# Kernel optimization log

Hardware: AMD Instinct MI355X
Metric: run time of the kernel (lower is better)

Reference implementation:

```python
import jax, jax.numpy as jnp
import numpy as np

# ---- fixed analysis filters (pywt_coeffs) ----
GL = np.array([0.05441584224308161, 0.3128715909144659, 0.6756307362980128, 0.5853546836548691, -0.015829105256023893, -0.2840155429624281, 0.00047248457399797254, 0.128747426620186, -0.01736930100202211, -0.04408825393106472, 0.013981027917015516, 0.008746094047015655, -0.00487035299301066, -0.0003917403729959771, 0.0006754494059985568, -0.00011747678400228192])
GH = np.array([-0.00011747678400228192, -0.0006754494059985568, -0.0003917403729959771, 0.00487035299301066, 0.008746094047015655, -0.013981027917015516, -0.04408825393106472, 0.01736930100202211, 0.128747426620186, -0.00047248457399797254, -0.2840155429624281, 0.015829105256023893, 0.5853546836548691, -0.6756307362980128, 0.3128715909144659, -0.05441584224308161])

M2 = 8          # fix(16*0.5), half filter length
A_CUBIC = -0.75 # PyTorch bicubic coefficient


def _ihilbert(x):
    # scipy.fftpack.ihilbert: Fourier coeff y_j = -1j*sign(j)*x_j, y_0 = 0
    n = x.shape[0]
    signs = np.sign(np.fft.fftfreq(n))
    return np.real(np.fft.ifft(np.fft.fft(x) * (-1j) * signs))


def setup_inputs() -> dict:
    key = jax.random.key(0)
    k1, k2 = jax.random.split(key)
    LL = jax.random.normal(k1, (8, 32, 256, 256), dtype=jnp.float32)
    Yh0 = jax.random.normal(k2, (8, 32, 3, 256, 256), dtype=jnp.float32)
    gl = jnp.asarray(GL, dtype=jnp.float32)
    gh = jnp.asarray(GH, dtype=jnp.float32)
    fl = jnp.asarray(_ihilbert(GL), dtype=jnp.float32)
    fh = jnp.asarray(_ihilbert(GH), dtype=jnp.float32)
    return {"LL": LL, "Yh0": Yh0, "gl": gl, "gh": gh, "fl": fl, "fh": fh}


def _reflect_idx(n):
    # reflect(arange(-m2, n+m2), -0.5, n-0.5) -> half-sample reflected indices, length n+2*M2
    x = jnp.arange(-M2, n + M2, dtype=jnp.float32)
    rng = jnp.float32(n)  # (n-0.5) - (-0.5)
    mod = jnp.mod(x + 0.5, 2.0 * rng)
    out = jnp.where(mod >= rng, 2.0 * rng - mod, mod) - 0.5
    return out.astype(jnp.int32)


def colfilter(X, h):
    # Faithful to original: reflect-pad gather along rows, then the original
    # _column_convolve accumulates X*h[idx] WITHOUT shifting (source bug), which
    # equals X_ext * sum(h); the centered crop recovers the original rows.
    r = X.shape[2]
    xe = _reflect_idx(r)
    Y = X[:, :, xe, :] * jnp.sum(h)
    return Y[:, :, M2:M2 + r, :]


def rowfilter(X, h):
    c = X.shape[3]
    xe = _reflect_idx(c)
    Y = X[:, :, :, xe] * jnp.sum(h)
    return Y[:, :, :, M2:M2 + c]


def _cubic_kernel(d):
    d = jnp.abs(d)
    w1 = ((A_CUBIC + 2.0) * d - (A_CUBIC + 3.0)) * d * d + 1.0
    w2 = ((A_CUBIC * d - 5.0 * A_CUBIC) * d + 8.0 * A_CUBIC) * d - 4.0 * A_CUBIC
    return jnp.where(d <= 1.0, w1, jnp.where(d < 2.0, w2, 0.0))


def _up2_axis(X, axis):
    # PyTorch nn.Upsample(scale_factor=2, mode='bicubic', align_corners=False)
    n = X.shape[axis]
    i = jnp.arange(2 * n, dtype=jnp.float32)
    src = 0.5 * i - 0.25                      # (i+0.5)*in/out - 0.5
    f = jnp.floor(src)
    offs = jnp.arange(-1, 3, dtype=jnp.float32)
    pos = f[:, None] + offs[None, :]          # [2n, 4] tap positions
    idx = jnp.clip(pos, 0, n - 1).astype(jnp.int32)
    w = _cubic_kernel(src[:, None] - pos)     # [2n, 4]
    Xg = jnp.take(X, idx.reshape(-1), axis=axis)
    new_shape = X.shape[:axis] + (2 * n, 4) + X.shape[axis + 1:]
    Xg = Xg.reshape(new_shape)
    wb = w.reshape((1,) * axis + (2 * n, 4) + (1,) * (X.ndim - axis - 1))
    return jnp.sum(Xg * wb, axis=axis + 1)


def upsample2(X):
    return _up2_axis(_up2_axis(X, 2), 3)


def _iqwt(LL, Yh0, gl, gh, fl, fh):
    LH, HL, HH = Yh0[:, :, 0], Yh0[:, :, 1], Yh0[:, :, 2]
    s = LL.shape[1] // 4
    sp = lambda T: (T[:, 0:s], T[:, s:2 * s], T[:, 2 * s:3 * s], T[:, 3 * s:4 * s])
    lglg, lflg, lglf, lflf = sp(LL)
    lghg, lfhg, lghf, lfhf = sp(LH)
    hglg, hflg, hglf, hflf = sp(HL)
    hghg, hfhg, hghf, hfhf = sp(HH)

    # first component
    lghg_f = rowfilter(lghg, gh)  # reused below (original code bug)
    t = upsample2(rowfilter(lglg, gl)) + upsample2(lghg_f)
    t1 = colfilter(t, gl)
    t = upsample2(rowfilter(hglg, gl)) + upsample2(rowfilter(hghg, gh))
    first = t1 + colfilter(t, gh)

    # second component (note: original uses lghg_f, not rowfilter(lfhg, gh))
    t = upsample2(rowfilter(lflg, gl)) + upsample2(lghg_f)
    t1 = colfilter(t, fl)
    t = upsample2(rowfilter(hflg, gl)) + upsample2(rowfilter(hfhg, gh))
    second = t1 + colfilter(t, fh)

    # third component
    t = upsample2(rowfilter(lglf, fl)) + upsample2(rowfilter(lghf, fh))
    t1 = colfilter(t, gl)
    t = upsample2(rowfilter(hglf, fl)) + upsample2(rowfilter(hghf, fh))
    third = t1 + colfilter(t, gh)

    # fourth component
    t = upsample2(rowfilter(lflf, fl)) + upsample2(rowfilter(lfhf, fh))
    t1 = colfilter(t, fl)
    t = upsample2(rowfilter(hflf, fl)) + upsample2(rowfilter(hfhf, fh))
    fourth = t1 + colfilter(t, fh)

    y = first + second + third + fourth
    return (y - jnp.min(y)) / (jnp.max(y) - jnp.min(y))


def reference(LL, Yh0, gl, gh, fl, fh):
    return _iqwt(LL, Yh0, gl, gh, fl, fh)
```

## Files before the change

kernel.cpp:

```cpp
#include <hip/hip_runtime.h>

constexpr int IT  = 36;
constexpr int ITP = 37;
constexpr int STP = 68;

#define W0 (-0.03515625f)
#define W1 ( 0.26171875f)
#define W2 ( 0.87890625f)
#define W3 (-0.10546875f)

typedef float vfloat4 __attribute__((ext_vector_type(4)));

template <typename F>
__device__ __forceinline__ void tile_pipeline(
    const float* __restrict__ src, int tx, int ty, int t,
    float (&sIn)[IT][ITP], float (&sT)[IT][STP],
    float a0, float a1, float a2, float a3, int b0, int g, F&& consume)
{
    const int rin0 = ty * 32 - 2;
    const int cin0 = tx * 32 - 2;

    for (int idx = t; idx < IT * IT; idx += 256) {
        int r  = idx / IT;
        int cc = idx - r * IT;
        int gr = min(max(rin0 + r, 0), 255);
        int gc = min(max(cin0 + cc, 0), 255);
        sIn[r][cc] = src[gr * 256 + gc];
    }
    __syncthreads();

    for (int r = t >> 4; r < IT; r += 16) {
        float x0 = sIn[r][2 * g + 0];
        float x1 = sIn[r][2 * g + 1];
        float x2 = sIn[r][2 * g + 2];
        float x3 = sIn[r][2 * g + 3];
        float x4 = sIn[r][2 * g + 4];
        float x5 = sIn[r][2 * g + 5];
        vfloat4 v;
        v.x = W0 * x0 + W1 * x1 + W2 * x2 + W3 * x3;
        v.y = W3 * x1 + W2 * x2 + W1 * x3 + W0 * x4;
        v.z = W0 * x1 + W1 * x2 + W2 * x3 + W3 * x4;
        v.w = W3 * x2 + W2 * x3 + W1 * x4 + W0 * x5;
        *(vfloat4*)&sT[r][4 * g] = v;
    }
    __syncthreads();

#pragma unroll
    for (int it = 0; it < 4; ++it) {
        const int base = b0 + 8 * it;
        vfloat4 q0 = *(const vfloat4*)&sT[base + 0][4 * g];
        vfloat4 q1 = *(const vfloat4*)&sT[base + 1][4 * g];
        vfloat4 q2 = *(const vfloat4*)&sT[base + 2][4 * g];
        vfloat4 q3 = *(const vfloat4*)&sT[base + 3][4 * g];
        vfloat4 v = a0 * q0 + a1 * q1 + a2 * q2 + a3 * q3;
        consume(it, v);
    }
}

__device__ __forceinline__ void block_minmax(int t, float& mn, float& mx) {
    for (int off = 32; off > 0; off >>= 1) {
        mn = fminf(mn, __shfl_down(mn, off, 64));
        mx = fmaxf(mx, __shfl_down(mx, off, 64));
    }
    __shared__ float wmn[4], wmx[4];
    const int wv = t >> 6;
    if ((t & 63) == 0) { wmn[wv] = mn; wmx[wv] = mx; }
    __syncthreads();
    mn = fminf(fminf(wmn[0], wmn[1]), fminf(wmn[2], wmn[3]));
    mx = fmaxf(fmaxf(wmx[0], wmx[1]), fmaxf(wmx[2], wmx[3]));
}

__global__ __launch_bounds__(256)
void qwt_pass1(const float* __restrict__ LL,
               float* __restrict__ pmin, float* __restrict__ pmax)
{
    __shared__ float sIn[IT][ITP];
    __shared__ float sT[IT][STP];

    const int t  = threadIdx.x;
    const int tx = blockIdx.x;
    const int ty = blockIdx.y;
    const int pl = blockIdx.z;
    const float* src = LL + (size_t)((pl >> 3) * 32 + (pl & 7)) * (256 * 256);

    const int g  = t & 15;
    const int rs = t >> 4;
    const int od = rs & 1;
    const int b0 = (rs >> 1) + od;
    const float a0 = od ? W3 : W0;
    const float a1 = od ? W2 : W1;
    const float a2 = od ? W1 : W2;
    const float a3 = od ? W0 : W3;

    float mn = 1e30f, mx = -1e30f;
    tile_pipeline(src, tx, ty, t, sIn, sT, a0, a1, a2, a3, b0, g,
        [&](int, vfloat4 v) {
            mn = fminf(mn, fminf(fminf(v.x, v.y), fminf(v.z, v.w)));
            mx = fmaxf(mx, fmaxf(fmaxf(v.x, v.y), fmaxf(v.z, v.w)));
        });

    block_minmax(t, mn, mx);
    if (t == 0) {
        const int p = (pl * 8 + ty) * 8 + tx;
        pmin[p] = mn;
        pmax[p] = mx;
    }
}

__global__ __launch_bounds__(256)
void qwt_reduce(const float* __restrict__ pmin,
                const float* __restrict__ pmax,
                float* __restrict__ res)
{
    const int t = threadIdx.x;
    float m = 1e30f, M = -1e30f;
#pragma unroll
    for (int k = 0; k < 16; ++k) {
        m = fminf(m, pmin[t + 256 * k]);
        M = fmaxf(M, pmax[t + 256 * k]);
    }
    block_minmax(t, m, M);
    if (t == 0) {
        res[0] = m;
        res[1] = 1.0f / (M - m);
    }
}

__global__ __launch_bounds__(256)
void qwt_pass2(const float* __restrict__ LL, float* __restrict__ out,
               const float* __restrict__ res)
{
    __shared__ float sIn[IT][ITP];
    __shared__ float sT[IT][STP];

    const float sub = res[0];
    const float scl = res[1];

    const int t  = threadIdx.x;
    const int tx = blockIdx.x;
    const int ty = blockIdx.y;
    const int pl = blockIdx.z;
    const float* src = LL + (size_t)((pl >> 3) * 32 + (pl & 7)) * (256 * 256);

    const int g  = t & 15;
    const int rs = t >> 4;
    const int od = rs & 1;
    const int b0 = (rs >> 1) + od;
    const float a0 = od ? W3 : W0;
    const float a1 = od ? W2 : W1;
    const float a2 = od ? W1 : W2;
    const float a3 = od ? W0 : W3;

    float* dst = out + (size_t)pl * (512 * 512)
               + (size_t)(ty * 64 + rs) * 512 + tx * 64 + 4 * g;

    tile_pipeline(src, tx, ty, t, sIn, sT, a0, a1, a2, a3, b0, g,
        [&](int it, vfloat4 v) {
            vfloat4 o = (v - sub) * scl;
            __builtin_nontemporal_store(o, (vfloat4*)(dst + (size_t)(16 * it) * 512));
        });
}

extern "C" void kernel_launch(void* const* d_in, const int* in_sizes, int n_in,
                              void* d_out, int out_size, void* d_ws, size_t ws_size,
                              hipStream_t stream)
{
    (void)in_sizes; (void)n_in; (void)out_size; (void)ws_size;
    const float* LL = (const float*)d_in[0];
    float* out      = (float*)d_out;

    float* pmin = (float*)d_ws;
    float* pmax = pmin + 4096;
    float* res  = pmin + 8192;

    dim3 grid(8, 8, 64);
    dim3 block(256);
    qwt_pass1<<<grid, block, 0, stream>>>(LL, pmin, pmax);
    qwt_reduce<<<dim3(1), block, 0, stream>>>(pmin, pmax, res);
    qwt_pass2<<<grid, block, 0, stream>>>(LL, out, res);
}
```

Before: 296.8 us.

## Store unnormalized upsampled output in first pass, normalize in place afterward

The first kernel now writes the raw upsampled tile to the output buffer while it computes per-block min/max. The second pass no longer reloads the input and recomputes the two-stage filter. Instead, a grid-stride elementwise kernel rescales the output buffer in place. This removes the duplicated input load and filter arithmetic, but the 64-plane 512x512 output now has to be read back and written a second time, which adds memory traffic.

```diff
diff --git a/kernel.cpp b/kernel.cpp
--- a/kernel.cpp
+++ b/kernel.cpp
@@ -71,8 +71,8 @@
 }
 
 __global__ __launch_bounds__(256)
-void qwt_pass1(const float* __restrict__ LL,
-               float* __restrict__ pmin, float* __restrict__ pmax)
+void qwt_up(const float* __restrict__ LL, float* __restrict__ out,
+            float* __restrict__ pmin, float* __restrict__ pmax)
 {
     __shared__ float sIn[IT][ITP];
     __shared__ float sT[IT][STP];
@@ -92,11 +92,15 @@
     const float a2 = od ? W1 : W2;
     const float a3 = od ? W0 : W3;
 
+    float* dst = out + (size_t)pl * (512 * 512)
+               + (size_t)(ty * 64 + rs) * 512 + tx * 64 + 4 * g;
+
     float mn = 1e30f, mx = -1e30f;
     tile_pipeline(src, tx, ty, t, sIn, sT, a0, a1, a2, a3, b0, g,
-        [&](int, vfloat4 v) {
+        [&](int it, vfloat4 v) {
             mn = fminf(mn, fminf(fminf(v.x, v.y), fminf(v.z, v.w)));
             mx = fmaxf(mx, fmaxf(fmaxf(v.x, v.y), fmaxf(v.z, v.w)));
+            *(vfloat4*)(dst + (size_t)(16 * it) * 512) = v;
         });
 
     block_minmax(t, mn, mx);
@@ -127,38 +131,20 @@
 }
 
 __global__ __launch_bounds__(256)
-void qwt_pass2(const float* __restrict__ LL, float* __restrict__ out,
-               const float* __restrict__ res)
+void qwt_norm(float* __restrict__ out, const float* __restrict__ res)
 {
-    __shared__ float sIn[IT][ITP];
-    __shared__ float sT[IT][STP];
-
     const float sub = res[0];
     const float scl = res[1];
 
-    const int t  = threadIdx.x;
-    const int tx = blockIdx.x;
-    const int ty = blockIdx.y;
-    const int pl = blockIdx.z;
-    const float* src = LL + (size_t)((pl >> 3) * 32 + (pl & 7)) * (256 * 256);
+    constexpr size_t N4 = (size_t)64 * 512 * 512 / 4;
+    vfloat4* p = (vfloat4*)out;
 
-    const int g  = t & 15;
-    const int rs = t >> 4;
-    const int od = rs & 1;
-    const int b0 = (rs >> 1) + od;
-    const float a0 = od ? W3 : W0;
-    const float a1 = od ? W2 : W1;
-    const float a2 = od ? W1 : W2;
-    const float a3 = od ? W0 : W3;
-
-    float* dst = out + (size_t)pl * (512 * 512)
-               + (size_t)(ty * 64 + rs) * 512 + tx * 64 + 4 * g;
-
-    tile_pipeline(src, tx, ty, t, sIn, sT, a0, a1, a2, a3, b0, g,
-        [&](int it, vfloat4 v) {
-            vfloat4 o = (v - sub) * scl;
-            __builtin_nontemporal_store(o, (vfloat4*)(dst + (size_t)(16 * it) * 512));
-        });
+    size_t i = (size_t)blockIdx.x * 256 + threadIdx.x;
+    const size_t stride = (size_t)gridDim.x * 256;
+    for (size_t k = i; k < N4; k += stride) {
+        vfloat4 v = p[k];
+        __builtin_nontemporal_store((v - sub) * scl, &p[k]);
+    }
 }
 
 extern "C" void kernel_launch(void* const* d_in, const int* in_sizes, int n_in,
@@ -173,9 +159,8 @@
     float* pmax = pmin + 4096;
     float* res  = pmin + 8192;
 
-    dim3 grid(8, 8, 64);
     dim3 block(256);
-    qwt_pass1<<<grid, block, 0, stream>>>(LL, pmin, pmax);
+    qwt_up<<<dim3(8, 8, 64), block, 0, stream>>>(LL, out, pmin, pmax);
     qwt_reduce<<<dim3(1), block, 0, stream>>>(pmin, pmax, res);
-    qwt_pass2<<<grid, block, 0, stream>>>(LL, out, res);
+    qwt_norm<<<dim3(2048), block, 0, stream>>>(out, res);
 }
```

Result: slower. 304.2 us (+2.5%).
